# Performance work log

Hardware: AMD Instinct MI355X
Metric: run time of the kernel (lower is better)

The kernel has to match this reference:

```python
import jax, jax.numpy as jnp
import numpy as np

B, S, D_IN, D_E, H = 512, 100, 300, 150, 2  # batch, patches, patch feat, embed half, heads
L = S + 1  # 101 tokens with class token
EPS = 1e-5


def setup_inputs() -> dict:
    key = jax.random.key(0)
    ks = jax.random.split(key, 12)
    r = lambda k, shp, s=0.02: (jax.random.normal(k, shp, jnp.float32) * s)
    return {
        "x": jax.random.normal(ks[0], (B, S, D_IN), jnp.float32),
        "Wp": r(ks[1], (D_IN, D_E)), "bp": jnp.zeros((D_E,), jnp.float32),
        "pos_table": r(ks[2], (L, D_E), 1.0),
        "class_embed": r(ks[3], (D_E,), 1.0),
        "Wq": r(ks[4], (H, 2 * D_E, 2 * D_E)),
        "Wk": r(ks[5], (H, 2 * D_E, 2 * D_E)),
        "Wv": r(ks[6], (H, 2 * D_E, 2 * D_E)),
        "bn1_g": jnp.ones((L,), jnp.float32), "bn1_b": jnp.zeros((L,), jnp.float32),
        "Wp1": r(ks[7], (900, 300)), "bp1": jnp.zeros((300,), jnp.float32),
        "bn2_g": jnp.ones((L,), jnp.float32), "bn2_b": jnp.zeros((L,), jnp.float32),
        "fc1_W": r(ks[8], (1200, 512)), "fc1_b": jnp.zeros((512,), jnp.float32),
        "fc2_W": r(ks[9], (512, 2)), "fc2_b": jnp.zeros((2,), jnp.float32),
    }


def _batchnorm(x, g, b):
    # torch BatchNorm1d(101) on [B, 101, F]: normalize per channel (dim 1) over (B, F), training-mode batch stats
    mean = jnp.mean(x, axis=(0, 2), keepdims=True)
    var = jnp.var(x, axis=(0, 2), keepdims=True)
    return (x - mean) * jax.lax.rsqrt(var + EPS) * g[None, :, None] + b[None, :, None]


def reference(x, Wp, bp, pos_table, class_embed, Wq, Wk, Wv, bn1_g, bn1_b,
              Wp1, bp1, bn2_g, bn2_b, fc1_W, fc1_b, fc2_W, fc2_b):
    h = jax.nn.relu(x @ Wp + bp)                                   # [B,100,150]
    cls = jnp.concatenate([jnp.broadcast_to(class_embed, (B, D_E)),
                           jnp.broadcast_to(pos_table[0], (B, D_E))], axis=-1)   # [B,300]
    tok = jnp.concatenate([h, jnp.broadcast_to(pos_table[1:], (B, S, D_E))], axis=-1)  # [B,100,300]
    z = jnp.concatenate([cls[:, None, :], tok], axis=1)            # [B,101,300]
    skip1 = jax.lax.stop_gradient(z)                               # x.clone().detach()

    # multi-head self-attention (per-head Q/K/V, no 1/sqrt(d) scaling, matching source)
    Q = jnp.einsum('bsd,hde->hbse', z, Wq)                         # [H,B,101,300]
    K = jnp.einsum('bsd,hde->hbse', z, Wk)
    V = jnp.einsum('bsd,hde->hbse', z, Wv)
    attn = jax.nn.softmax(jnp.einsum('hbse,hbte->hbst', Q, K), axis=-1)  # [H,B,101,101]
    o = jnp.einsum('hbst,hbte->hbse', attn, V)                     # [H,B,101,300]
    msa = jnp.transpose(o, (1, 2, 0, 3)).reshape(B, L, H * 2 * D_E)  # concat heads -> [B,101,600]

    y = _batchnorm(msa, bn1_g, bn1_b)
    y = jnp.concatenate([y, skip1], axis=-1)                       # [B,101,900]
    skip2 = jax.lax.stop_gradient(y)
    y = jax.nn.relu(y @ Wp1 + bp1)                                 # [B,101,300]
    y = _batchnorm(y, bn2_g, bn2_b)
    y = jnp.concatenate([y, skip2], axis=-1)                       # [B,101,1200]
    out = (y[:, 0, :] @ fc1_W + fc1_b) @ fc2_W + fc2_b             # [B,2]
    return out
```

## Files before the change

### kernel.cpp

```cpp
#include <hip/hip_runtime.h>
#include <hip/hip_fp16.h>
#include <math.h>

#define BB 512
#define SS 100
#define DE 150
#define DM 300
#define LL 101
#define NH 2

typedef _Float16 f16x8 __attribute__((ext_vector_type(8)));
typedef float f32x4 __attribute__((ext_vector_type(4)));

#define WS_CLS    0
#define WS_QK     320
#define WS_S0     960
#define WS_CPOS   964
#define WS_CVEC   1200
#define WS_COLSUM 1536
#define WS_CST0   1856
#define WS_STATS  1860
#define WS_G      2176
#define WS_P3     5248
#define WS_PART1  14336
#define WS_PART2  15360
#define WS_MSA    16384
#define WS_Y1     (WS_MSA + 512*600)
#define WS_WPF    477184
#define WS_WVF    502784
#define WS_ZB16   605184
#define WS_Q0P    769024

__global__ void kC1(const float* __restrict__ pos, const float* __restrict__ cle,
                    const float* __restrict__ Wq, const float* __restrict__ Wp1,
                    const float* __restrict__ Wp, const float* __restrict__ Wv,
                    const float* __restrict__ f1W, const float* __restrict__ f2W,
                    const float* __restrict__ f1b, const float* __restrict__ f2b,
                    float* __restrict__ ws) {
  __shared__ float cls[DM];
  int b = blockIdx.x, tid = threadIdx.x;
  if (b < 35) {
    for (int i = tid; i < DM; i += 256) cls[i] = (i < DE) ? cle[i] : pos[i - DE];
    __syncthreads();
  }
  if (b < 20) {
    int p = b >> 1, h = b & 1;
    const float* wqh = Wq + h * DM * DM;
    int d0 = p * 30;
    for (int e = tid; e < DM; e += 256) {
      float acc = 0.f;
#pragma unroll
      for (int d = 0; d < 30; ++d) acc += cls[d0 + d] * wqh[(d0 + d) * DM + e];
      ws[WS_Q0P + p * 600 + h * 300 + e] = acc;
    }
  } else if (b < 35) {
    int kb = b - 20;
    for (int n = tid; n < DM; n += 256) {
      float cs = 0.f, cv = 0.f;
      for (int k = kb * 60; k < kb * 60 + 60; ++k) {
        float w = Wp1[k * 300 + n];
        if (k < 600) cs += w; else cv += cls[k - 600] * w;
      }
      ws[WS_P3 + kb * 600 + n] = cs;
      ws[WS_P3 + kb * 600 + 300 + n] = cv;
    }
  } else if (b == 35) {
    for (int i = tid; i < DM; i += 256)
      ws[WS_CLS + i] = (i < DE) ? cle[i] : pos[i - DE];
  } else if (b < 111) {
    int wave = tid >> 6, lane = tid & 63;
    int kbase = (b - 36) * 16 + wave * 4;
#pragma unroll
    for (int j = 0; j < 4; ++j) {
      int k = kbase + j;
      const float* r = f1W + k * 512;
      float a0 = 0.f, a1 = 0.f;
      for (int m = lane; m < 512; m += 64) {
        float a = r[m];
        float2 f2 = *(const float2*)&f2W[m * 2];
        a0 += a * f2.x; a1 += a * f2.y;
      }
      for (int o = 32; o; o >>= 1) { a0 += __shfl_xor(a0, o); a1 += __shfl_xor(a1, o); }
      if (!lane) { ws[WS_G + k * 2] = a0; ws[WS_G + k * 2 + 1] = a1; }
    }
  } else if (b == 111) {
    int wave = tid >> 6, lane = tid & 63;
    if (wave < 2) {
      float acc = 0.f;
      for (int m = lane; m < 512; m += 64) acc += f1b[m] * f2W[m * 2 + wave];
      for (int o = 32; o; o >>= 1) acc += __shfl_xor(acc, o);
      if (!lane) ws[WS_CST0 + wave] = f2b[wave] + acc;
    }
  } else if (b < 137) {
    int idx = (b - 112) * 256 + tid;
    int kq = idx / 160, n = idx % 160;
    f16x8 pk;
#pragma unroll
    for (int j = 0; j < 8; ++j) {
      int k = kq * 8 + j;
      float v = (k < DM && n < DE) ? Wp[k * DE + n] : 0.f;
      pk[j] = (_Float16)v;
    }
    *(f16x8*)((char*)ws + (size_t)WS_WPF * 4 + (size_t)idx * 16) = pk;
  } else {
    int idx = (b - 137) * 256 + tid;
    int h = idx / 12800, rem = idx % 12800;
    int kq = rem / 320, n = rem % 320;
    f16x8 pk;
#pragma unroll
    for (int j = 0; j < 8; ++j) {
      int k = kq * 8 + j;
      float v = (k < DM && n < DM) ? Wv[h * DM * DM + k * DM + n] : 0.f;
      pk[j] = (_Float16)v;
    }
    *(f16x8*)((char*)ws + (size_t)WS_WVF * 4 + (size_t)idx * 16) = pk;
  }
}

__global__ void kC2p(const float* __restrict__ Wk, const float* __restrict__ bp1,
                     float* __restrict__ ws) {
  int b = blockIdx.x, tid = threadIdx.x;
  if (b == 150) {
    for (int n = tid; n < DM; n += 256) {
      float cs = 0.f, cv = bp1[n];
      for (int p = 0; p < 15; ++p) {
        cs += ws[WS_P3 + p * 600 + n];
        cv += ws[WS_P3 + p * 600 + 300 + n];
      }
      ws[WS_COLSUM + n] = cs;
      ws[WS_CVEC + n] = cv;
    }
    return;
  }
  __shared__ float q0s[NH * DM];
  for (int i = tid; i < NH * DM; i += 256) {
    float s = 0.f;
#pragma unroll
    for (int p = 0; p < 10; ++p) s += ws[WS_Q0P + p * 600 + i];
    q0s[i] = s;
  }
  __syncthreads();
  int wave = tid >> 6, lane = tid & 63;
  int idx = b * 4 + wave;
  int h = idx / DM, d = idx % DM;
  const float* w = Wk + h * DM * DM + d * DM;
  const float* q = q0s + h * DM;
  float acc = 0.f;
  for (int e = lane; e < DM; e += 64) acc += w[e] * q[e];
  for (int o = 32; o; o >>= 1) acc += __shfl_xor(acc, o);
  if (!lane) ws[WS_QK + idx] = acc;
}

__global__ void kC3(const float* __restrict__ pos, float* __restrict__ ws) {
  int b = blockIdx.x, tid = threadIdx.x;
  int wave = tid >> 6, lane = tid & 63;
  if (b < 50) {
    int idx = b * 4 + wave;
    int tt = idx >> 1, h = idx & 1;
    const float* pr = pos + (tt + 1) * DE;
    const float* qk = ws + WS_QK + h * DM + DE;
    float acc = 0.f;
    for (int j = lane; j < DE; j += 64) acc += pr[j] * qk[j];
    for (int o = 32; o; o >>= 1) acc += __shfl_xor(acc, o);
    if (!lane) ws[WS_CPOS + idx] = acc;
  } else {
    if (wave < NH) {
      float acc = 0.f;
      for (int d = lane; d < DM; d += 64) acc += ws[WS_CLS + d] * ws[WS_QK + wave * DM + d];
      for (int o = 32; o; o >>= 1) acc += __shfl_xor(acc, o);
      if (!lane) ws[WS_S0 + wave] = acc;
    }
  }
}

__launch_bounds__(512, 4)
__global__ void kA(const float* __restrict__ x, const float* __restrict__ bp,
                   const float* __restrict__ pos, float* __restrict__ ws) {
  __shared__ __align__(16) char smem[41600];
  __half (*hb)[DE + 2] = (__half(*)[DE + 2])smem;
  _Float16* wpt0 = (_Float16*)(smem);
  _Float16* xs0  = (_Float16*)(smem + 10240);
  _Float16* wpt1 = (_Float16*)(smem + 18240);
  _Float16* xs1  = (_Float16*)(smem + 28480);
  float* aux = (float*)(smem + 36480);

  int b = blockIdx.x, tid = threadIdx.x;
  int w = tid >> 6, lane = tid & 63;
  int l16 = lane & 15, lg = lane >> 4;
  int wm = w >> 2, wn = w & 3;
  int nnt = (wn < 3) ? 3 : 1;
  int nt0 = (wn < 3) ? wn * 3 : 9;

  const float* xb = x + b * (SS * DM);
  const char* wpf = (const char*)ws + (size_t)WS_WPF * 4;
  int rowl[4];
#pragma unroll
  for (int mt = 0; mt < 4; ++mt) {
    int r = wm * 64 + mt * 16 + l16;
    rowl[mt] = (r < SS) ? r : (SS - 1);
  }

  f32x4 acc[4][3];
#pragma unroll
  for (int mt = 0; mt < 4; ++mt)
#pragma unroll
    for (int nti = 0; nti < 3; ++nti) acc[mt][nti] = (f32x4){0.f, 0.f, 0.f, 0.f};

  float xrA[4][2], xrB[4][2];
  float4 waA, wb2A, waB, wb2B;

#define XLOAD2(S, XR)                                                          \
  { int kc_ = (S) * 32;                                                        \
    _Pragma("unroll")                                                          \
    for (int i_ = 0; i_ < 4; ++i_) {                                           \
      int t_ = tid + 512 * i_;                                                 \
      if (t_ < 1600) {                                                         \
        int r_ = t_ >> 4, c_ = t_ & 15, k_ = kc_ + 2 * c_;                     \
        if (k_ + 1 < DM) {                                                     \
          float2 v_ = *(const float2*)(xb + r_ * DM + k_);                     \
          XR[i_][0] = v_.x; XR[i_][1] = v_.y;                                  \
        } else {                                                               \
          XR[i_][0] = (k_ < DM) ? xb[r_ * DM + k_] : 0.f;                      \
          XR[i_][1] = 0.f;                                                     \
        } } } }

#define XWRITE2(XP, XR)                                                        \
  { _Pragma("unroll")                                                          \
    for (int i_ = 0; i_ < 4; ++i_) {                                           \
      int t_ = tid + 512 * i_;                                                 \
      if (t_ < 1600) {                                                         \
        int r_ = t_ >> 4, c_ = t_ & 15;                                        \
        *(__half2*)((char*)(XP) + r_ * 80 + c_ * 4) =                          \
            __floats2half2_rn(XR[i_][0], XR[i_][1]);                           \
      } } }

#define WLOAD2(S, WA, WB)                                                      \
  { const char* s_ = wpf + (size_t)(S) * 10240;                                \
    WA = *(const float4*)(s_ + tid * 16);                                      \
    if (tid < 128) WB = *(const float4*)(s_ + (tid + 512) * 16); }

#define WWRITE2(WP, WA, WB)                                                    \
  { *(float4*)((char*)(WP) + tid * 16) = WA;                                   \
    if (tid < 128) *(float4*)((char*)(WP) + (tid + 512) * 16) = WB; }

  XLOAD2(0, xrA); WLOAD2(0, waA, wb2A);
  XWRITE2(xs0, xrA); WWRITE2(wpt0, waA, wb2A);
  XLOAD2(1, xrB); WLOAD2(1, waB, wb2B);
  __syncthreads();

  for (int s = 0; s < 10; ++s) {
    _Float16* wc = (s & 1) ? wpt1 : wpt0;
    _Float16* xc = (s & 1) ? xs1 : xs0;
    _Float16* wnx = (s & 1) ? wpt0 : wpt1;
    _Float16* xnx = (s & 1) ? xs0 : xs1;
    if (s < 8) {
      if (s & 1) { XLOAD2(s + 2, xrB); WLOAD2(s + 2, waB, wb2B); }
      else       { XLOAD2(s + 2, xrA); WLOAD2(s + 2, waA, wb2A); }
    }
    f16x8 Bf[3];
#pragma unroll
    for (int nti = 0; nti < 3; ++nti)
      if (nti < nnt)
        Bf[nti] = *(const f16x8*)(wc + ((lg * 160 + (nt0 + nti) * 16 + l16) * 8));
#pragma unroll
    for (int mt = 0; mt < 4; ++mt) {
      f16x8 Af = *(const f16x8*)(xc + rowl[mt] * 40 + lg * 8);
#pragma unroll
      for (int nti = 0; nti < 3; ++nti)
        if (nti < nnt)
          acc[mt][nti] = __builtin_amdgcn_mfma_f32_16x16x32_f16(Af, Bf[nti], acc[mt][nti], 0, 0, 0);
    }
    if (s < 9) {
      if (s & 1) { XWRITE2(xnx, xrA); WWRITE2(wnx, waA, wb2A); }
      else       { XWRITE2(xnx, xrB); WWRITE2(wnx, waB, wb2B); }
    }
    __syncthreads();
  }

#pragma unroll
  for (int nti = 0; nti < 3; ++nti) {
    if (nti < nnt) {
      int col = (nt0 + nti) * 16 + l16;
      float bpv = (col < DE) ? bp[col] : 0.f;
#pragma unroll
      for (int mt = 0; mt < 4; ++mt) {
        int rbase = wm * 64 + mt * 16 + lg * 4;
        f32x4 v = acc[mt][nti];
#pragma unroll
        for (int reg = 0; reg < 4; ++reg) {
          int row = rbase + reg;
          if (row < SS && col < DE) {
            float hv = v[reg] + bpv;
            hb[row][col] = __float2half(hv > 0.f ? hv : 0.f);
          }
        }
      }
    }
  }
  for (int i = tid; i < DM; i += 512) {
    aux[i] = ws[WS_QK + (i / DE) * DM + (i % DE)];
    aux[DM + i] = ws[WS_CLS + i];
  }
  __syncthreads();

  if (tid < NH * SS) {
    int hh = tid / SS, tt = tid % SS;
    const __half2* hr = (const __half2*)&hb[tt][0];
    const float* qr = &aux[hh * DE];
    float sa = 0.f, sb = 0.f;
    for (int j2 = 0; j2 < 74; j2 += 2) {
      float2 h0 = __half22float2(hr[j2]);
      float2 q0 = *(const float2*)&qr[2 * j2];
      float2 h1 = __half22float2(hr[j2 + 1]);
      float2 q1 = *(const float2*)&qr[2 * j2 + 2];
      sa += h0.x * q0.x + h0.y * q0.y;
      sb += h1.x * q1.x + h1.y * q1.y;
    }
    {
      float2 h0 = __half22float2(hr[74]);
      float2 q0 = *(const float2*)&qr[148];
      sa += h0.x * q0.x + h0.y * q0.y;
    }
    aux[600 + hh * LL + tt + 1] = sa + sb + ws[WS_CPOS + tt * NH + hh];
  } else if (tid < NH * SS + NH) {
    int hh = tid - NH * SS;
    aux[600 + hh * LL] = ws[WS_S0 + hh];
  }
  __syncthreads();

  if (w < NH) {
    float v0 = aux[600 + w * LL + lane];
    float v1 = (lane + 64 < LL) ? aux[600 + w * LL + lane + 64] : -1e30f;
    float m = fmaxf(v0, v1);
    for (int o = 32; o; o >>= 1) m = fmaxf(m, __shfl_xor(m, o));
    float e0 = expf(v0 - m);
    float e1 = (lane + 64 < LL) ? expf(v1 - m) : 0.f;
    float s = e0 + e1;
    for (int o = 32; o; o >>= 1) s += __shfl_xor(s, o);
    float inv = 1.f / s;
    aux[802 + w * LL + lane] = e0 * inv;
    if (lane + 64 < LL) aux[802 + w * LL + lane + 64] = e1 * inv;
  }
  __syncthreads();

  __half* zb16 = (__half*)((char*)ws + (size_t)WS_ZB16 * 4);
  for (int o = tid; o < NH * DM; o += 512) {
    int hh = o / DM, d = o % DM;
    const float* p = &aux[802 + hh * LL];
    float accA = p[0] * aux[DM + d], accB = 0.f;
    if (d < DE) {
      for (int t = 1; t < 100; t += 2) {
        accA += p[t] * __half2float(hb[t - 1][d]);
        accB += p[t + 1] * __half2float(hb[t][d]);
      }
    } else {
      int dd = d - DE;
      for (int t = 1; t < 100; t += 2) {
        accA += p[t] * pos[t * DE + dd];
        accB += p[t + 1] * pos[(t + 1) * DE + dd];
      }
    }
    zb16[((size_t)hh * 512 + b) * 320 + d] = __float2half(accA + accB);
  }
  if (tid < 40) {
    int hh = tid / 20, dd = 300 + tid % 20;
    zb16[((size_t)hh * 512 + b) * 320 + dd] = __float2half(0.f);
  }
}

__launch_bounds__(512, 4)
__global__ void kV(float* __restrict__ ws) {
  __shared__ float shp[2][8];
  int blk = blockIdx.x;
  int mtile = blk >> 2, nb = (blk >> 1) & 1, h = blk & 1;
  int tid = threadIdx.x;
  int w = tid >> 6, lane = tid & 63;
  int l16 = lane & 15, lg = lane >> 4;
  int wm = w >> 2, wn = w & 3;
  int nnt = (wn < 3) ? 3 : 1;
  int nt0 = (wn < 3) ? wn * 3 : 9;
  int mbase = mtile * 128;

  const __half* zb16 = (const __half*)((const char*)ws + (size_t)WS_ZB16 * 4) + (size_t)h * 512 * 320;
  const __half* wvf  = (const __half*)((const char*)ws + (size_t)WS_WVF * 4) + (size_t)h * 40 * 320 * 8;

  int brow[4];
#pragma unroll
  for (int mt = 0; mt < 4; ++mt) brow[mt] = mbase + wm * 64 + mt * 16 + l16;

  f32x4 acc[4][3];
#pragma unroll
  for (int mt = 0; mt < 4; ++mt)
#pragma unroll
    for (int nti = 0; nti < 3; ++nti) acc[mt][nti] = (f32x4){0.f, 0.f, 0.f, 0.f};

  for (int s = 0; s < 10; ++s) {
    f16x8 Bf[3];
#pragma unroll
    for (int nti = 0; nti < 3; ++nti)
      if (nti < nnt) {
        int n = nb * 160 + (nt0 + nti) * 16 + l16;
        Bf[nti] = *(const f16x8*)&wvf[((size_t)(s * 4 + lg) * 320 + n) * 8];
      }
#pragma unroll
    for (int mt = 0; mt < 4; ++mt) {
      f16x8 Af = *(const f16x8*)&zb16[(size_t)brow[mt] * 320 + s * 32 + lg * 8];
#pragma unroll
      for (int nti = 0; nti < 3; ++nti)
        if (nti < nnt)
          acc[mt][nti] = __builtin_amdgcn_mfma_f32_16x16x32_f16(Af, Bf[nti], acc[mt][nti], 0, 0, 0);
    }
  }

  float s_ = 0.f, ss_ = 0.f;
#pragma unroll
  for (int nti = 0; nti < 3; ++nti) {
    if (nti < nnt) {
      int col = nb * 160 + (nt0 + nti) * 16 + l16;
      if (col < DM) {
#pragma unroll
        for (int mt = 0; mt < 4; ++mt) {
          int rbase = mbase + wm * 64 + mt * 16 + lg * 4;
          f32x4 v = acc[mt][nti];
#pragma unroll
          for (int reg = 0; reg < 4; ++reg) {
            int row = rbase + reg;
            float val = v[reg];
            ws[WS_MSA + row * 600 + h * DM + col] = val;
            s_ += val; ss_ += val * val;
          }
        }
      }
    }
  }
  for (int o = 32; o; o >>= 1) { s_ += __shfl_xor(s_, o); ss_ += __shfl_xor(ss_, o); }
  if (!lane) { shp[0][w] = s_; shp[1][w] = ss_; }
  __syncthreads();
  if (!tid) {
    float S = 0.f, SS2 = 0.f;
    for (int i = 0; i < 8; ++i) { S += shp[0][i]; SS2 += shp[1][i]; }
    ws[WS_PART1 + blk * 2] = S;
    ws[WS_PART1 + blk * 2 + 1] = SS2;
  }
}

__launch_bounds__(512)
__global__ void k5(const float* __restrict__ Wp1, const float* __restrict__ g1,
                   const float* __restrict__ b1, float* __restrict__ ws) {
  __shared__ float ab[2][600];
  __shared__ float part[2][2][300];
  __shared__ float sh[2][8];
  __shared__ float s_a1, s_b1;
  int b0 = blockIdx.x * 2, tid = threadIdx.x;
  int wv = tid >> 6, ln = tid & 63;
  for (int i = tid; i < 1200; i += 512) ab[i / 600][i % 600] = ws[WS_MSA + b0 * 600 + i];
  {
    float s = 0.f, ss = 0.f;
    if (tid < 16) { s = ws[WS_PART1 + tid * 2]; ss = ws[WS_PART1 + tid * 2 + 1]; }
    for (int o = 32; o; o >>= 1) { s += __shfl_xor(s, o); ss += __shfl_xor(ss, o); }
    if (!ln) { sh[0][wv] = s; sh[1][wv] = ss; }
  }
  __syncthreads();
  if (!tid) {
    float S = 0.f, SS2 = 0.f;
    for (int i = 0; i < 8; ++i) { S += sh[0][i]; SS2 += sh[1][i]; }
    float n = (float)(BB * 600);
    float mean = S / n, var = SS2 / n - mean * mean;
    float a = (1.f / sqrtf(var + 1e-5f)) * g1[0];
    s_a1 = a; s_b1 = b1[0] - a * mean;
    if (blockIdx.x == 0) { ws[WS_STATS + 0] = a; ws[WS_STATS + 1] = s_b1; }
  }
  __syncthreads();
  int g = tid >> 8, t = tid & 255;
  int kbeg = g * 300, kend = kbeg + 300;
  for (int n = t; n < 300; n += 256) {
    float a0 = 0.f, a1v = 0.f;
    for (int k = kbeg; k < kend; ++k) {
      float wq = Wp1[k * 300 + n];
      a0 += ab[0][k] * wq;
      a1v += ab[1][k] * wq;
    }
    part[g][0][n] = a0;
    part[g][1][n] = a1v;
  }
  __syncthreads();
  float a1 = s_a1, beta1 = s_b1;
  float s2 = 0.f, ss2 = 0.f;
  for (int n = tid; n < 300; n += 512) {
    float c = beta1 * ws[WS_COLSUM + n] + ws[WS_CVEC + n];
    float v0 = a1 * (part[0][0][n] + part[1][0][n]) + c;
    float v1 = a1 * (part[0][1][n] + part[1][1][n]) + c;
    v0 = v0 > 0.f ? v0 : 0.f;
    v1 = v1 > 0.f ? v1 : 0.f;
    ws[WS_Y1 + b0 * 300 + n] = v0;
    ws[WS_Y1 + (b0 + 1) * 300 + n] = v1;
    s2 += v0 + v1; ss2 += v0 * v0 + v1 * v1;
  }
  for (int o = 32; o; o >>= 1) { s2 += __shfl_xor(s2, o); ss2 += __shfl_xor(ss2, o); }
  if (!ln) { sh[0][wv] = s2; sh[1][wv] = ss2; }
  __syncthreads();
  if (!tid) {
    float S = 0.f, SS2 = 0.f;
    for (int i = 0; i < 8; ++i) { S += sh[0][i]; SS2 += sh[1][i]; }
    ws[WS_PART2 + blockIdx.x * 2] = S;
    ws[WS_PART2 + blockIdx.x * 2 + 1] = SS2;
  }
}

__launch_bounds__(256)
__global__ void k7(const float* __restrict__ g2, const float* __restrict__ b2,
                   float* __restrict__ out, const float* __restrict__ ws) {
  __shared__ float Gs[2400];
  __shared__ float sh[2][4];
  __shared__ float cc[4];
  int tid = threadIdx.x, wv = tid >> 6, ln = tid & 63;
  for (int i = tid; i < 2400; i += 256) Gs[i] = ws[WS_G + i];
  {
    float s = ws[WS_PART2 + tid * 2], ss = ws[WS_PART2 + tid * 2 + 1];
    for (int o = 32; o; o >>= 1) { s += __shfl_xor(s, o); ss += __shfl_xor(ss, o); }
    if (!ln) { sh[0][wv] = s; sh[1][wv] = ss; }
  }
  __syncthreads();
  if (!tid) {
    float S = 0.f, SS2 = 0.f;
    for (int i = 0; i < 4; ++i) { S += sh[0][i]; SS2 += sh[1][i]; }
    float n = (float)(BB * 300);
    float mean = S / n, var = SS2 / n - mean * mean;
    float a = (1.f / sqrtf(var + 1e-5f)) * g2[0];
    cc[0] = a; cc[1] = b2[0] - a * mean;
  }
  __syncthreads();
  if (tid < 2) {
    int c = tid;
    float sg1 = 0.f, sg2 = 0.f, sg3 = 0.f;
    for (int k = 0; k < 300; ++k) sg1 += Gs[k * 2 + c];
    for (int k = 300; k < 900; ++k) sg2 += Gs[k * 2 + c];
    for (int j = 0; j < 300; ++j) sg3 += ws[WS_CLS + j] * Gs[(900 + j) * 2 + c];
    cc[2 + c] = ws[WS_CST0 + c] + sg3 + cc[1] * sg1 + ws[WS_STATS + 1] * sg2;
  }
  __syncthreads();
  int b = blockIdx.x * 4 + wv;
  float a1 = ws[WS_STATS + 0], a2 = cc[0];
  const float* y1 = ws + WS_Y1 + b * 300;
  const float* ms = ws + WS_MSA + b * 600;
  float o0 = 0.f, o1 = 0.f, p0 = 0.f, p1 = 0.f;
  for (int k = ln; k < 300; k += 64) { float v = y1[k]; o0 += v * Gs[k * 2]; o1 += v * Gs[k * 2 + 1]; }
  for (int j = ln; j < 600; j += 64) { float v = ms[j]; p0 += v * Gs[(300 + j) * 2]; p1 += v * Gs[(300 + j) * 2 + 1]; }
  for (int o = 32; o; o >>= 1) {
    o0 += __shfl_xor(o0, o); o1 += __shfl_xor(o1, o);
    p0 += __shfl_xor(p0, o); p1 += __shfl_xor(p1, o);
  }
  if (!ln) {
    out[b * 2] = a2 * o0 + a1 * p0 + cc[2];
    out[b * 2 + 1] = a2 * o1 + a1 * p1 + cc[3];
  }
}

extern "C" void kernel_launch(void* const* d_in, const int* in_sizes, int n_in,
                              void* d_out, int out_size, void* d_ws, size_t ws_size,
                              hipStream_t stream) {
  const float* x    = (const float*)d_in[0];
  const float* Wp   = (const float*)d_in[1];
  const float* bp   = (const float*)d_in[2];
  const float* pos  = (const float*)d_in[3];
  const float* cle  = (const float*)d_in[4];
  const float* Wq   = (const float*)d_in[5];
  const float* Wk   = (const float*)d_in[6];
  const float* Wv   = (const float*)d_in[7];
  const float* bn1g = (const float*)d_in[8];
  const float* bn1b = (const float*)d_in[9];
  const float* Wp1  = (const float*)d_in[10];
  const float* bp1  = (const float*)d_in[11];
  const float* bn2g = (const float*)d_in[12];
  const float* bn2b = (const float*)d_in[13];
  const float* f1W  = (const float*)d_in[14];
  const float* f1b  = (const float*)d_in[15];
  const float* f2W  = (const float*)d_in[16];
  const float* f2b  = (const float*)d_in[17];
  float* ws = (float*)d_ws;
  float* out = (float*)d_out;

  hipLaunchKernelGGL(kC1, dim3(237), dim3(256), 0, stream, pos, cle, Wq, Wp1, Wp, Wv, f1W, f2W, f1b, f2b, ws);
  hipLaunchKernelGGL(kC2p, dim3(151), dim3(256), 0, stream, Wk, bp1, ws);
  hipLaunchKernelGGL(kC3, dim3(51), dim3(256), 0, stream, pos, ws);
  hipLaunchKernelGGL(kA, dim3(512), dim3(512), 0, stream, x, bp, pos, ws);
  hipLaunchKernelGGL(kV, dim3(16), dim3(512), 0, stream, ws);
  hipLaunchKernelGGL(k5, dim3(256), dim3(512), 0, stream, Wp1, bn1g, bn1b, ws);
  hipLaunchKernelGGL(k7, dim3(128), dim3(256), 0, stream, bn2g, bn2b, out, ws);
}
```

Measured before the change: 127.0 us.

## Load patch-projection weight fragments directly from global and triple-buffer x tiles

The kernel no longer stages the fp16 projection weight tiles through shared memory. Each wave now reads its B fragments straight from the global workspace, which removes the weight store to LDS and its register staging. The x tiles move to a three-slot LDS ring, and the hb buffer gets its own region instead of aliasing the staging area. The LDS footprint grows, so launch bounds drop from 4 to 2 blocks per CU. That lowers occupancy and makes the MFMA loop wait on global or L2 latency for the weights.

Measured after the change: 128.8 us. No clear change (+1.5%).

```diff
diff --git a/kernel.cpp b/kernel.cpp
--- a/kernel.cpp
+++ b/kernel.cpp
@@ -173,16 +173,13 @@
   }
 }
 
-__launch_bounds__(512, 4)
+__launch_bounds__(512, 2)
 __global__ void kA(const float* __restrict__ x, const float* __restrict__ bp,
                    const float* __restrict__ pos, float* __restrict__ ws) {
-  __shared__ __align__(16) char smem[41600];
-  __half (*hb)[DE + 2] = (__half(*)[DE + 2])smem;
-  _Float16* wpt0 = (_Float16*)(smem);
-  _Float16* xs0  = (_Float16*)(smem + 10240);
-  _Float16* wpt1 = (_Float16*)(smem + 18240);
-  _Float16* xs1  = (_Float16*)(smem + 28480);
-  float* aux = (float*)(smem + 36480);
+  __shared__ __align__(16) char smem[59520];
+  _Float16* xsb = (_Float16*)smem;
+  __half (*hb)[DE + 2] = (__half(*)[DE + 2])(smem + 24000);
+  float* aux = (float*)(smem + 54400);
 
   int b = blockIdx.x, tid = threadIdx.x;
   int w = tid >> 6, lane = tid & 63;
@@ -192,7 +189,7 @@
   int nt0 = (wn < 3) ? wn * 3 : 9;
 
   const float* xb = x + b * (SS * DM);
-  const char* wpf = (const char*)ws + (size_t)WS_WPF * 4;
+  const _Float16* wpfh = (const _Float16*)((const char*)ws + (size_t)WS_WPF * 4);
   int rowl[4];
 #pragma unroll
   for (int mt = 0; mt < 4; ++mt) {
@@ -207,7 +204,6 @@
     for (int nti = 0; nti < 3; ++nti) acc[mt][nti] = (f32x4){0.f, 0.f, 0.f, 0.f};
 
   float xrA[4][2], xrB[4][2];
-  float4 waA, wb2A, waB, wb2B;
 
 #define XLOAD2(S, XR)                                                          \
   { int kc_ = (S) * 32;                                                        \
@@ -234,45 +230,34 @@
             __floats2half2_rn(XR[i_][0], XR[i_][1]);                           \
       } } }
 
-#define WLOAD2(S, WA, WB)                                                      \
-  { const char* s_ = wpf + (size_t)(S) * 10240;                                \
-    WA = *(const float4*)(s_ + tid * 16);                                      \
-    if (tid < 128) WB = *(const float4*)(s_ + (tid + 512) * 16); }
-
-#define WWRITE2(WP, WA, WB)                                                    \
-  { *(float4*)((char*)(WP) + tid * 16) = WA;                                   \
-    if (tid < 128) *(float4*)((char*)(WP) + (tid + 512) * 16) = WB; }
-
-  XLOAD2(0, xrA); WLOAD2(0, waA, wb2A);
-  XWRITE2(xs0, xrA); WWRITE2(wpt0, waA, wb2A);
-  XLOAD2(1, xrB); WLOAD2(1, waB, wb2B);
-  __syncthreads();
-
+  XLOAD2(0, xrA);
+  XWRITE2(xsb, xrA);
+  XLOAD2(1, xrB);
+  __syncthreads();
+
+  _Float16* bufs[3] = {xsb, xsb + 4000, xsb + 8000};
   for (int s = 0; s < 10; ++s) {
-    _Float16* wc = (s & 1) ? wpt1 : wpt0;
-    _Float16* xc = (s & 1) ? xs1 : xs0;
-    _Float16* wnx = (s & 1) ? wpt0 : wpt1;
-    _Float16* xnx = (s & 1) ? xs0 : xs1;
+    _Float16* rd = bufs[s % 3];
+    _Float16* wr = bufs[(s + 1) % 3];
     if (s < 8) {
-      if (s & 1) { XLOAD2(s + 2, xrB); WLOAD2(s + 2, waB, wb2B); }
-      else       { XLOAD2(s + 2, xrA); WLOAD2(s + 2, waA, wb2A); }
+      if (s & 1) { XLOAD2(s + 2, xrB); } else { XLOAD2(s + 2, xrA); }
     }
     f16x8 Bf[3];
 #pragma unroll
     for (int nti = 0; nti < 3; ++nti)
       if (nti < nnt)
-        Bf[nti] = *(const f16x8*)(wc + ((lg * 160 + (nt0 + nti) * 16 + l16) * 8));
+        Bf[nti] = *(const f16x8*)(wpfh +
+            ((size_t)(s * 4 + lg) * 160 + (nt0 + nti) * 16 + l16) * 8);
 #pragma unroll
     for (int mt = 0; mt < 4; ++mt) {
-      f16x8 Af = *(const f16x8*)(xc + rowl[mt] * 40 + lg * 8);
+      f16x8 Af = *(const f16x8*)(rd + rowl[mt] * 40 + lg * 8);
 #pragma unroll
       for (int nti = 0; nti < 3; ++nti)
         if (nti < nnt)
           acc[mt][nti] = __builtin_amdgcn_mfma_f32_16x16x32_f16(Af, Bf[nti], acc[mt][nti], 0, 0, 0);
     }
     if (s < 9) {
-      if (s & 1) { XWRITE2(xnx, xrA); WWRITE2(wnx, waA, wb2A); }
-      else       { XWRITE2(xnx, xrB); WWRITE2(wnx, waB, wb2B); }
+      if (s & 1) { XWRITE2(wr, xrA); } else { XWRITE2(wr, xrB); }
     }
     __syncthreads();
   }
```
